# Kernel optimization log

Measured on AMD Instinct MI355X. Metric: run time of the kernel, lower is better.

Reference implementation:

```python
import jax, jax.numpy as jnp
import numpy as np

B, N, F, H = 1, 8192, 512, 64
NEG_BIAS = -9.0  # GAT adjacency bias for non-edges


def setup_inputs() -> dict:
    key = jax.random.key(0)
    ks = jax.random.split(key, 6)
    features = jax.random.normal(ks[0], (B, N, F), dtype=jnp.float32)
    edge = jax.random.uniform(ks[1], (B, N, N)) < 0.02
    bias_mat = jnp.where(edge, 0.0, NEG_BIAS).astype(jnp.float32)
    W = jax.random.normal(ks[2], (F, H), dtype=jnp.float32) * 0.05   # 1x1 conv, no bias
    a1 = jax.random.normal(ks[3], (H, 1), dtype=jnp.float32) * 0.05  # f_1 1x1 conv
    b1 = jnp.zeros((1,), dtype=jnp.float32)
    a2 = jax.random.normal(ks[4], (H, 1), dtype=jnp.float32) * 0.05  # f_2 1x1 conv
    b2 = jnp.zeros((1,), dtype=jnp.float32)
    return {"features": features, "bias_mat": bias_mat, "W": W,
            "a1": a1, "b1": b1, "a2": a2, "b2": b2}


def reference(features, bias_mat, W, a1, b1, a2, b2):
    # 1x1 conv projection (no bias): [B,N,F] @ [F,H] -> [B,N,H]
    fts = jnp.einsum('bnf,fh->bnh', features, W)
    # per-node scalar attention terms: [B,N,1]
    f1 = jnp.einsum('bnh,ho->bno', fts, a1) + b1
    f2 = jnp.einsum('bnh,ho->bno', fts, a2) + b2
    # additive pairwise logits: [B,N,N]
    logits = f1 + jnp.swapaxes(f2, 1, 2)
    # masked softmax over neighbors, then (as written in source) add bias again
    coefs = jax.nn.softmax(jax.nn.relu(logits) + bias_mat, axis=-1) + bias_mat
    # weighted aggregation: [B,N,N] @ [B,N,H] -> [B,N,H]
    vals = jnp.einsum('bmn,bnh->bmh', coefs, fts)
    return jax.nn.elu(vals)
```

## Files before the change

### kernel.cpp

```cpp
#include <hip/hip_runtime.h>
#include <math.h>

#define N 8192
#define FDIM 512
#define H 64
#define MAXE 512

__global__ __launch_bounds__(256) void k_fts(const float* __restrict__ feat,
                                             const float* __restrict__ W,
                                             const float* __restrict__ a1v,
                                             const float* __restrict__ b1v,
                                             const float* __restrict__ a2v,
                                             const float* __restrict__ b2v,
                                             float* __restrict__ fts,
                                             float* __restrict__ f1,
                                             float* __restrict__ f2,
                                             float* __restrict__ T) {
    __shared__ float Af[32][65];
    __shared__ float Bf[64][64];
    __shared__ float colred[16][64];
    const int t = threadIdx.x;
    const int row0 = blockIdx.x * 32;
    const int hq = (t & 15) * 4;
    const int rq = (t >> 4) * 2;
    float acc[2][4] = {};
    for (int k0 = 0; k0 < FDIM; k0 += 64) {
#pragma unroll
        for (int i = 0; i < 2; ++i) {
            int l = t + i * 256;
            int r = l >> 4;
            int c4 = (l & 15) * 4;
            float4 av = *(const float4*)&feat[(size_t)(row0 + r) * FDIM + k0 + c4];
            Af[r][c4 + 0] = av.x; Af[r][c4 + 1] = av.y;
            Af[r][c4 + 2] = av.z; Af[r][c4 + 3] = av.w;
        }
#pragma unroll
        for (int i = 0; i < 4; ++i) {
            int l = t + i * 256;
            int r = l >> 4;
            int c4 = (l & 15) * 4;
            *(float4*)&Bf[r][c4] = *(const float4*)&W[(size_t)(k0 + r) * H + c4];
        }
        __syncthreads();
#pragma unroll 8
        for (int kk = 0; kk < 64; ++kk) {
            float a0 = Af[rq][kk];
            float a1_ = Af[rq + 1][kk];
            float4 b = *(const float4*)&Bf[kk][hq];
            acc[0][0] += a0 * b.x;  acc[0][1] += a0 * b.y;
            acc[0][2] += a0 * b.z;  acc[0][3] += a0 * b.w;
            acc[1][0] += a1_ * b.x; acc[1][1] += a1_ * b.y;
            acc[1][2] += a1_ * b.z; acc[1][3] += a1_ * b.w;
        }
        __syncthreads();
    }
#pragma unroll
    for (int j = 0; j < 2; ++j) {
        float4 v = make_float4(acc[j][0], acc[j][1], acc[j][2], acc[j][3]);
        *(float4*)&fts[(size_t)(row0 + rq + j) * H + hq] = v;
    }
    float pa1[4], pa2[4];
#pragma unroll
    for (int i = 0; i < 4; ++i) { pa1[i] = a1v[hq + i]; pa2[i] = a2v[hq + i]; }
#pragma unroll
    for (int j = 0; j < 2; ++j) {
        float s1 = acc[j][0] * pa1[0] + acc[j][1] * pa1[1] + acc[j][2] * pa1[2] + acc[j][3] * pa1[3];
        float s2 = acc[j][0] * pa2[0] + acc[j][1] * pa2[1] + acc[j][2] * pa2[2] + acc[j][3] * pa2[3];
#pragma unroll
        for (int o = 8; o; o >>= 1) { s1 += __shfl_xor(s1, o); s2 += __shfl_xor(s2, o); }
        if ((t & 15) == 0) {
            f1[row0 + rq + j] = s1 + b1v[0];
            f2[row0 + rq + j] = s2 + b2v[0];
        }
    }
#pragma unroll
    for (int i = 0; i < 4; ++i)
        colred[t >> 4][hq + i] = acc[0][i] + acc[1][i];
    __syncthreads();
    if (t < H) {
        float s = 0.f;
#pragma unroll
        for (int g = 0; g < 16; ++g) s += colred[g][t];
        atomicAdd(&T[t], s);
    }
}

__global__ __launch_bounds__(256) void k_main(const float* __restrict__ bias,
                                              const float* __restrict__ fts,
                                              const float* __restrict__ f1g,
                                              const float* __restrict__ f2g,
                                              const float* __restrict__ T,
                                              float* __restrict__ out) {
    __shared__ int   listN[MAXE];
    __shared__ float redW[16][64];
    __shared__ float redF[16][64];
    __shared__ float redE[16];
    __shared__ int wbase[4];
    __shared__ int s_cnt;
    const int t = threadIdx.x;
    const int m = blockIdx.x;
    const int lane = t & 63;
    const int w = t >> 6;
    const float f1m = f1g[m];

    const float4* brow = (const float4*)(bias + (size_t)m * N);
    float4 r[8];
#pragma unroll
    for (int i = 0; i < 8; ++i) r[i] = brow[t + i * 256];
    int c = 0;
#pragma unroll
    for (int i = 0; i < 8; ++i)
        c += (r[i].x == 0.f) + (r[i].y == 0.f) + (r[i].z == 0.f) + (r[i].w == 0.f);
    int sc = c;
#pragma unroll
    for (int o = 1; o < 64; o <<= 1) {
        int u = __shfl_up(sc, o);
        if (lane >= o) sc += u;
    }
    if (lane == 63) wbase[w] = sc;
    __syncthreads();
    int base = 0;
#pragma unroll
    for (int ww = 0; ww < 4; ++ww) if (ww < w) base += wbase[ww];
    int pos = base + sc - c;
#pragma unroll
    for (int i = 0; i < 8; ++i) {
        int nb = (t + i * 256) * 4;
        if (r[i].x == 0.f) { if (pos < MAXE) listN[pos] = nb;     ++pos; }
        if (r[i].y == 0.f) { if (pos < MAXE) listN[pos] = nb + 1; ++pos; }
        if (r[i].z == 0.f) { if (pos < MAXE) listN[pos] = nb + 2; ++pos; }
        if (r[i].w == 0.f) { if (pos < MAXE) listN[pos] = nb + 3; ++pos; }
    }
    if (t == 255) s_cnt = pos;
    __syncthreads();
    const int cnt = s_cnt < MAXE ? s_cnt : MAXE;

    const int g = t >> 4;
    const int h4 = (t & 15) * 4;
    float4 aW = make_float4(0.f, 0.f, 0.f, 0.f);
    float4 aF = make_float4(0.f, 0.f, 0.f, 0.f);
    float aE = 0.f;
    int e = g;
    float4 v0 = make_float4(0.f, 0.f, 0.f, 0.f);
    float ff0 = 0.f;
    if (e < cnt) {
        int n = listN[e];
        v0 = *(const float4*)&fts[(size_t)n * H + h4];
        ff0 = f2g[n];
    }
    while (e < cnt) {
        int e1 = e + 16;
        float4 v1 = make_float4(0.f, 0.f, 0.f, 0.f);
        float ff1 = 0.f;
        if (e1 < cnt) {
            int n1 = listN[e1];
            v1 = *(const float4*)&fts[(size_t)n1 * H + h4];
            ff1 = f2g[n1];
        }
        float ee = __expf(fmaxf(f1m + ff0, 0.f));
        aW.x += ee * v0.x; aW.y += ee * v0.y; aW.z += ee * v0.z; aW.w += ee * v0.w;
        aF.x += v0.x;      aF.y += v0.y;      aF.z += v0.z;      aF.w += v0.w;
        aE += ee;
        v0 = v1; ff0 = ff1; e = e1;
    }
    *(float4*)&redW[g][h4] = aW;
    *(float4*)&redF[g][h4] = aF;
    if ((t & 15) == 0) redE[g] = aE;
    __syncthreads();

    if (t < H) {
        float eW = 0.f, eF = 0.f, eE = 0.f;
#pragma unroll
        for (int s = 0; s < 16; ++s) { eW += redW[s][t]; eF += redF[s][t]; eE += redE[s]; }
        float S = (cnt > 0) ? eW / eE : 0.f;
        float val = S - 9.0f * (T[t] - eF);
        out[(size_t)m * H + t] = val > 0.f ? val : expm1f(val);
    }
}

extern "C" void kernel_launch(void* const* d_in, const int* in_sizes, int n_in,
                              void* d_out, int out_size, void* d_ws, size_t ws_size,
                              hipStream_t stream) {
    const float* feat = (const float*)d_in[0];
    const float* bias = (const float*)d_in[1];
    const float* W    = (const float*)d_in[2];
    const float* a1   = (const float*)d_in[3];
    const float* b1   = (const float*)d_in[4];
    const float* a2   = (const float*)d_in[5];
    const float* b2   = (const float*)d_in[6];
    float* out = (float*)d_out;

    float* ws  = (float*)d_ws;
    float* fts = ws;
    float* f1  = fts + (size_t)N * H;
    float* f2  = f1 + N;
    float* T   = f2 + N;

    hipMemsetAsync(T, 0, H * sizeof(float), stream);
    hipLaunchKernelGGL(k_fts,  dim3(N / 32), dim3(256), 0, stream,
                       feat, W, a1, b1, a2, b2, fts, f1, f2, T);
    hipLaunchKernelGGL(k_main, dim3(N), dim3(256), 0, stream,
                       bias, fts, f1, f2, T, out);
}
```

Before: 401.0 us.

## Assign one wavefront per attention row and transpose feature tile in LDS

The main kernel now gives each 64-lane wavefront its own output row, with four rows per block. It builds that row's neighbor list with wave-local scans over four chunks and accumulates one hidden column per lane, so no block-level syncs or shared-memory reductions are needed. The projection kernel stores the feature tile transposed so each thread reads two rows with one float2 LDS load. In exchange, each wave streams its 32KB bias row in four serial chunks, which may reduce memory-level parallelism per wave, and the gathers become scalar per lane.

```diff
diff --git a/kernel.cpp b/kernel.cpp
--- a/kernel.cpp
+++ b/kernel.cpp
@@ -16,7 +16,7 @@
                                              float* __restrict__ f1,
                                              float* __restrict__ f2,
                                              float* __restrict__ T) {
-    __shared__ float Af[32][65];
+    __shared__ float At[64][34];
     __shared__ float Bf[64][64];
     __shared__ float colred[16][64];
     const int t = threadIdx.x;
@@ -31,8 +31,8 @@
             int r = l >> 4;
             int c4 = (l & 15) * 4;
             float4 av = *(const float4*)&feat[(size_t)(row0 + r) * FDIM + k0 + c4];
-            Af[r][c4 + 0] = av.x; Af[r][c4 + 1] = av.y;
-            Af[r][c4 + 2] = av.z; Af[r][c4 + 3] = av.w;
+            At[c4 + 0][r] = av.x; At[c4 + 1][r] = av.y;
+            At[c4 + 2][r] = av.z; At[c4 + 3][r] = av.w;
         }
 #pragma unroll
         for (int i = 0; i < 4; ++i) {
@@ -44,13 +44,12 @@
         __syncthreads();
 #pragma unroll 8
         for (int kk = 0; kk < 64; ++kk) {
-            float a0 = Af[rq][kk];
-            float a1_ = Af[rq + 1][kk];
+            float2 a = *(const float2*)&At[kk][rq];
             float4 b = *(const float4*)&Bf[kk][hq];
-            acc[0][0] += a0 * b.x;  acc[0][1] += a0 * b.y;
-            acc[0][2] += a0 * b.z;  acc[0][3] += a0 * b.w;
-            acc[1][0] += a1_ * b.x; acc[1][1] += a1_ * b.y;
-            acc[1][2] += a1_ * b.z; acc[1][3] += a1_ * b.w;
+            acc[0][0] += a.x * b.x; acc[0][1] += a.x * b.y;
+            acc[0][2] += a.x * b.z; acc[0][3] += a.x * b.w;
+            acc[1][0] += a.y * b.x; acc[1][1] += a.y * b.y;
+            acc[1][2] += a.y * b.z; acc[1][3] += a.y * b.w;
         }
         __syncthreads();
     }
@@ -91,91 +90,75 @@
                                               const float* __restrict__ f2g,
                                               const float* __restrict__ T,
                                               float* __restrict__ out) {
-    __shared__ int   listN[MAXE];
-    __shared__ float redW[16][64];
-    __shared__ float redF[16][64];
-    __shared__ float redE[16];
-    __shared__ int wbase[4];
-    __shared__ int s_cnt;
+    __shared__ int listAll[4][MAXE];
     const int t = threadIdx.x;
-    const int m = blockIdx.x;
+    const int w = t >> 6;
     const int lane = t & 63;
-    const int w = t >> 6;
+    const int m = blockIdx.x * 4 + w;
+    int* myList = listAll[w];
     const float f1m = f1g[m];
+    const float4* brow = (const float4*)(bias + (size_t)m * N);
 
-    const float4* brow = (const float4*)(bias + (size_t)m * N);
-    float4 r[8];
+    int total = 0;
 #pragma unroll
-    for (int i = 0; i < 8; ++i) r[i] = brow[t + i * 256];
-    int c = 0;
+    for (int ch = 0; ch < 4; ++ch) {
+        float4 r[8];
 #pragma unroll
-    for (int i = 0; i < 8; ++i)
-        c += (r[i].x == 0.f) + (r[i].y == 0.f) + (r[i].z == 0.f) + (r[i].w == 0.f);
-    int sc = c;
+        for (int j = 0; j < 8; ++j) r[j] = brow[ch * 512 + j * 64 + lane];
+        int c = 0;
 #pragma unroll
-    for (int o = 1; o < 64; o <<= 1) {
-        int u = __shfl_up(sc, o);
-        if (lane >= o) sc += u;
+        for (int j = 0; j < 8; ++j)
+            c += (r[j].x == 0.f) + (r[j].y == 0.f) + (r[j].z == 0.f) + (r[j].w == 0.f);
+        int sc = c;
+#pragma unroll
+        for (int o = 1; o < 64; o <<= 1) {
+            int u = __shfl_up(sc, o);
+            if (lane >= o) sc += u;
+        }
+        int pos = total + sc - c;
+#pragma unroll
+        for (int j = 0; j < 8; ++j) {
+            int nb = (ch * 512 + j * 64 + lane) * 4;
+            if (r[j].x == 0.f && pos < MAXE) myList[pos++] = nb;
+            if (r[j].y == 0.f && pos < MAXE) myList[pos++] = nb + 1;
+            if (r[j].z == 0.f && pos < MAXE) myList[pos++] = nb + 2;
+            if (r[j].w == 0.f && pos < MAXE) myList[pos++] = nb + 3;
+        }
+        total += __shfl(sc, 63);
     }
-    if (lane == 63) wbase[w] = sc;
-    __syncthreads();
-    int base = 0;
+    const int cnt = total < MAXE ? total : MAXE;
+
+    float accW = 0.f, accF = 0.f, accE = 0.f;
+    int e = 0;
+    for (; e + 8 <= cnt; e += 8) {
+        int n[8];
 #pragma unroll
-    for (int ww = 0; ww < 4; ++ww) if (ww < w) base += wbase[ww];
-    int pos = base + sc - c;
+        for (int j = 0; j < 8; ++j) n[j] = myList[e + j];
+        float fv[8], vv[8];
 #pragma unroll
-    for (int i = 0; i < 8; ++i) {
-        int nb = (t + i * 256) * 4;
-        if (r[i].x == 0.f) { if (pos < MAXE) listN[pos] = nb;     ++pos; }
-        if (r[i].y == 0.f) { if (pos < MAXE) listN[pos] = nb + 1; ++pos; }
-        if (r[i].z == 0.f) { if (pos < MAXE) listN[pos] = nb + 2; ++pos; }
-        if (r[i].w == 0.f) { if (pos < MAXE) listN[pos] = nb + 3; ++pos; }
+        for (int j = 0; j < 8; ++j) {
+            fv[j] = f2g[n[j]];
+            vv[j] = fts[(size_t)n[j] * H + lane];
+        }
+#pragma unroll
+        for (int j = 0; j < 8; ++j) {
+            float ee = __expf(fmaxf(f1m + fv[j], 0.f));
+            accW += ee * vv[j];
+            accF += vv[j];
+            accE += ee;
+        }
     }
-    if (t == 255) s_cnt = pos;
-    __syncthreads();
-    const int cnt = s_cnt < MAXE ? s_cnt : MAXE;
-
-    const int g = t >> 4;
-    const int h4 = (t & 15) * 4;
-    float4 aW = make_float4(0.f, 0.f, 0.f, 0.f);
-    float4 aF = make_float4(0.f, 0.f, 0.f, 0.f);
-    float aE = 0.f;
-    int e = g;
-    float4 v0 = make_float4(0.f, 0.f, 0.f, 0.f);
-    float ff0 = 0.f;
-    if (e < cnt) {
-        int n = listN[e];
-        v0 = *(const float4*)&fts[(size_t)n * H + h4];
-        ff0 = f2g[n];
+    for (; e < cnt; ++e) {
+        int n = myList[e];
+        float ee = __expf(fmaxf(f1m + f2g[n], 0.f));
+        float vv = fts[(size_t)n * H + lane];
+        accW += ee * vv;
+        accF += vv;
+        accE += ee;
     }
-    while (e < cnt) {
-        int e1 = e + 16;
-        float4 v1 = make_float4(0.f, 0.f, 0.f, 0.f);
-        float ff1 = 0.f;
-        if (e1 < cnt) {
-            int n1 = listN[e1];
-            v1 = *(const float4*)&fts[(size_t)n1 * H + h4];
-            ff1 = f2g[n1];
-        }
-        float ee = __expf(fmaxf(f1m + ff0, 0.f));
-        aW.x += ee * v0.x; aW.y += ee * v0.y; aW.z += ee * v0.z; aW.w += ee * v0.w;
-        aF.x += v0.x;      aF.y += v0.y;      aF.z += v0.z;      aF.w += v0.w;
-        aE += ee;
-        v0 = v1; ff0 = ff1; e = e1;
-    }
-    *(float4*)&redW[g][h4] = aW;
-    *(float4*)&redF[g][h4] = aF;
-    if ((t & 15) == 0) redE[g] = aE;
-    __syncthreads();
-
-    if (t < H) {
-        float eW = 0.f, eF = 0.f, eE = 0.f;
-#pragma unroll
-        for (int s = 0; s < 16; ++s) { eW += redW[s][t]; eF += redF[s][t]; eE += redE[s]; }
-        float S = (cnt > 0) ? eW / eE : 0.f;
-        float val = S - 9.0f * (T[t] - eF);
-        out[(size_t)m * H + t] = val > 0.f ? val : expm1f(val);
-    }
+    float S = (cnt > 0) ? accW / accE : 0.f;
+    float val = S - 9.0f * (T[lane] - accF);
+    out[(size_t)m * H + lane] = val > 0.f ? val : expm1f(val);
 }
 
 extern "C" void kernel_launch(void* const* d_in, const int* in_sizes, int n_in,
@@ -199,6 +182,6 @@
     hipMemsetAsync(T, 0, H * sizeof(float), stream);
     hipLaunchKernelGGL(k_fts,  dim3(N / 32), dim3(256), 0, stream,
                        feat, W, a1, b1, a2, b2, fts, f1, f2, T);
-    hipLaunchKernelGGL(k_main, dim3(N), dim3(256), 0, stream,
+    hipLaunchKernelGGL(k_main, dim3(N / 4), dim3(256), 0, stream,
                        bias, fts, f1, f2, T, out);
 }
```

New measurement: 420.5 us. +4.9%, slower.
